# Kernel optimization log

Measured on AMD Instinct MI355X. Metric: run time of the kernel, lower is better.

Reference implementation:

```python
import jax, jax.numpy as jnp
import numpy as np

B, T, F, H, O = 64, 2048, 128, 512, 4
G = 4 * H  # gates: i, f, g, o (PyTorch order)


def setup_inputs() -> dict:
    key = jax.random.key(0)
    ks = jax.random.split(key, 12)
    s = 1.0 / np.sqrt(H)  # PyTorch LSTM init scale
    return {
        "x": jax.random.normal(ks[0], (B, T, F), dtype=jnp.float32),
        "W_ih_l0": jax.random.uniform(ks[1], (G, F), jnp.float32, -s, s),
        "W_hh_l0": jax.random.uniform(ks[2], (G, H), jnp.float32, -s, s),
        "b_ih_l0": jax.random.uniform(ks[3], (G,), jnp.float32, -s, s),
        "b_hh_l0": jax.random.uniform(ks[4], (G,), jnp.float32, -s, s),
        "W_ih_l1": jax.random.uniform(ks[5], (G, H), jnp.float32, -s, s),
        "W_hh_l1": jax.random.uniform(ks[6], (G, H), jnp.float32, -s, s),
        "b_ih_l1": jax.random.uniform(ks[7], (G,), jnp.float32, -s, s),
        "b_hh_l1": jax.random.uniform(ks[8], (G,), jnp.float32, -s, s),
        "W_out": jax.random.uniform(ks[9], (O, H), jnp.float32, -s, s),
        "b_out": jax.random.uniform(ks[10], (O,), jnp.float32, -s, s),
    }


def lstm_layer(x_seq, W_ih, W_hh, b_ih, b_hh):
    # x_seq: [B, T, Fin] -> (h_seq [B, T, H], h_final [B, H])
    b = x_seq.shape[0]
    h_dim = W_hh.shape[1]
    # Precompute input projections for all timesteps in one big GEMM.
    x_proj = jnp.einsum('btf,gf->btg', x_seq, W_ih) + b_ih + b_hh  # [B, T, 4H]

    def step(carry, xp_t):
        h, c = carry
        gates = xp_t + h @ W_hh.T  # [B, 4H]
        i, f, g, o = jnp.split(gates, 4, axis=-1)
        i = jax.nn.sigmoid(i)
        f = jax.nn.sigmoid(f)
        g = jnp.tanh(g)
        o = jax.nn.sigmoid(o)
        c = f * c + i * g
        h = o * jnp.tanh(c)
        return (h, c), h

    h0 = jnp.zeros((b, h_dim), x_seq.dtype)
    c0 = jnp.zeros((b, h_dim), x_seq.dtype)
    (hT, _), hs = jax.lax.scan(step, (h0, c0), jnp.swapaxes(x_proj, 0, 1))
    return jnp.swapaxes(hs, 0, 1), hT


def reference(x, W_ih_l0, W_hh_l0, b_ih_l0, b_hh_l0,
              W_ih_l1, W_hh_l1, b_ih_l1, b_hh_l1, W_out, b_out):
    h0_seq, h0_final = lstm_layer(x, W_ih_l0, W_hh_l0, b_ih_l0, b_hh_l0)
    _, h1_final = lstm_layer(h0_seq, W_ih_l1, W_hh_l1, b_ih_l1, b_hh_l1)
    # hn = stack([h0_final, h1_final]); relu(hn); linear applied to hn[0]
    hn0 = jax.nn.relu(h0_final)  # [B, H]
    out = hn0 @ W_out.T + b_out  # [B, 4]
    return out
```

## Files before the change

### kernel.cpp

```cpp
#include <hip/hip_runtime.h>
#include <hip/hip_bf16.h>
#include <cstdint>
#include <cstddef>


#define B_ 64
#define T_ 2048
#define F_ 128
#define H_ 512

#define NBLK 128
#define NTHR 256

#define ACT_STRIDE 1280
#define SMEM_SZ (16 * ACT_STRIDE)
#define HSLOT (B_ * H_)

typedef __bf16 bf16;
typedef __bf16 bf16x4 __attribute__((ext_vector_type(4)));
typedef __bf16 bf16x8 __attribute__((ext_vector_type(8)));
typedef float f32x4 __attribute__((ext_vector_type(4)));
typedef unsigned int u32;
typedef u32 u32x2 __attribute__((ext_vector_type(2)));
typedef u32 u32x4 __attribute__((ext_vector_type(4)));

static __device__ __forceinline__ float sigm(float v) {
  return __builtin_amdgcn_rcpf(1.f + __expf(-v));
}
static __device__ __forceinline__ float tanh_f(float v) {
  float a = fminf(fabsf(v), 20.f);
  float e = __expf(-2.f * a);
  float t = 1.f - 2.f * e * __builtin_amdgcn_rcpf(1.f + e);
  return copysignf(t, v);
}
static __device__ __forceinline__ u32 bf16bits(float f) {
  bf16 b = (bf16)f;
  unsigned short us;
  __builtin_memcpy(&us, &b, 2);
  return (u32)us;
}
static __device__ __forceinline__ u32 min4(u32x4 v) {
  u32 a = v[0] < v[1] ? v[0] : v[1];
  u32 b = v[2] < v[3] ? v[2] : v[3];
  return a < b ? a : b;
}

__global__ void __launch_bounds__(NTHR) prep_kernel(u32* hbuf) {
  int idx = blockIdx.x * blockDim.x + threadIdx.x;
  if (idx < 2 * HSLOT) hbuf[idx] = 0u;
}

__global__ void __launch_bounds__(NTHR) xconv_kernel(
    const float* __restrict__ x, bf16* __restrict__ xbf) {
  const int b = blockIdx.x;
  const int t0 = blockIdx.y * 256;
  const int f2 = threadIdx.x & 63;
  const int tq = threadIdx.x >> 6;
  const int rg = b >> 4, row = b & 15;
  for (int i = 0; i < 64; ++i) {
    int t = t0 + i * 4 + tq;
    float2 xv = *(const float2*)(x + ((size_t)b * T_ + t) * F_ + 2 * f2);
    u32 w = bf16bits(xv.x) | (bf16bits(xv.y) << 16);
    *(u32*)((char*)xbf + ((((size_t)t * 4 + rg) * 16 + row) * 128 + 2 * f2) * 2) = w;
  }
}

__global__ void __launch_bounds__(NTHR, 1) lstm_kernel(
    const float* __restrict__ x,
    const float* __restrict__ Wih,
    const float* __restrict__ Whh,
    const float* __restrict__ bih,
    const float* __restrict__ bhh,
    u32* __restrict__ hbuf,
    float* __restrict__ hf32,
    const bf16* __restrict__ xbf)
{
  __shared__ __align__(16) char smem[SMEM_SZ];

  const int tid = threadIdx.x;
  const int bid = blockIdx.x;
  const int rg = bid >> 5;
  const int jg = bid & 31;
  const int row0 = rg * 16;
  const int j0 = jg * 16;

  const int lane = tid & 63;
  const int wave = tid >> 6;
  const int fr = lane & 15;
  const int kg = lane >> 4;

  bf16x8 wfrag[20];
  {
    const int G = (fr >> 2) * H_ + j0 + wave * 4 + (fr & 3);
    const float* sih = Wih + (size_t)G * F_;
    const float* shh = Whh + (size_t)G * H_;
    #pragma unroll
    for (int kk = 0; kk < 20; ++kk) {
      const float* s = (kk < 4) ? (sih + kk * 32 + kg * 8)
                                : (shh + (kk - 4) * 32 + kg * 8);
      float4 f0 = *(const float4*)s;
      float4 f1 = *(const float4*)(s + 4);
      bf16x8 w = { (bf16)f0.x, (bf16)f0.y, (bf16)f0.z, (bf16)f0.w,
                   (bf16)f1.x, (bf16)f1.y, (bf16)f1.z, (bf16)f1.w };
      wfrag[kk] = w;
    }
  }

  const int jcol = j0 + wave * 4 + kg;
  const float bi_ = bih[0 * H_ + jcol] + bhh[0 * H_ + jcol];
  const float bf_ = bih[1 * H_ + jcol] + bhh[1 * H_ + jcol];
  const float bg_ = bih[2 * H_ + jcol] + bhh[2 * H_ + jcol];
  const float bo_ = bih[3 * H_ + jcol] + bhh[3 * H_ + jcol];

  const int prow = tid >> 4;
  const int pw = tid & 15;
  const int r0x = tid >> 5;
  const int c40 = tid & 31;
  const float* xp0 = x + (size_t)(row0 + r0x) * T_ * F_ + c40 * 4;
  const float* xp1 = x + (size_t)(row0 + r0x + 8) * T_ * F_ + c40 * 4;
  const int xw0 = r0x * ACT_STRIDE + ((8 * c40) ^ ((r0x & 7) << 4));
  const int xw1 = (r0x + 8) * ACT_STRIDE + ((8 * c40) ^ (((r0x + 8) & 7) << 4));
  const int xw = prow * ACT_STRIDE + ((pw * 16) ^ ((prow & 7) << 4));

  const char* bbase = smem + fr * ACT_STRIDE;
  const int bmask = (fr & 7) << 4;

  float c_state = 0.f;
  int budget = 1 << 22;

  for (int t = 0; t < T_; ++t) {
    if (xbf) {
      u32x4 xv = *(const u32x4*)((const char*)xbf
                  + ((size_t)t * 4 + rg) * 4096 + tid * 16);
      *(u32x4*)(smem + xw) = xv;
    } else {
      float4 xv0 = *(const float4*)(xp0 + (size_t)t * F_);
      float4 xv1 = *(const float4*)(xp1 + (size_t)t * F_);
      bf16x4 b0 = { (bf16)xv0.x, (bf16)xv0.y, (bf16)xv0.z, (bf16)xv0.w };
      bf16x4 b1 = { (bf16)xv1.x, (bf16)xv1.y, (bf16)xv1.z, (bf16)xv1.w };
      *(bf16x4*)(smem + xw0) = b0;
      *(bf16x4*)(smem + xw1) = b1;
    }
    __syncthreads();

    u32x4 v0, v1, v2, v3, v4, v5, v6, v7;
    const u32* hb = hbuf + (size_t)(t & 1) * HSLOT + (size_t)(row0 + prow) * H_ + 4 * pw;
    asm volatile("global_load_dwordx4 %0, %1, off sc0 sc1"              : "=v"(v0) : "v"(hb));
    asm volatile("global_load_dwordx4 %0, %1, off offset:256 sc0 sc1"   : "=v"(v1) : "v"(hb));
    asm volatile("global_load_dwordx4 %0, %1, off offset:512 sc0 sc1"   : "=v"(v2) : "v"(hb));
    asm volatile("global_load_dwordx4 %0, %1, off offset:768 sc0 sc1"   : "=v"(v3) : "v"(hb));
    asm volatile("global_load_dwordx4 %0, %1, off offset:1024 sc0 sc1"  : "=v"(v4) : "v"(hb));
    asm volatile("global_load_dwordx4 %0, %1, off offset:1280 sc0 sc1"  : "=v"(v5) : "v"(hb));
    asm volatile("global_load_dwordx4 %0, %1, off offset:1536 sc0 sc1"  : "=v"(v6) : "v"(hb));
    asm volatile("global_load_dwordx4 %0, %1, off offset:1792 sc0 sc1"  : "=v"(v7) : "v"(hb));
    __builtin_amdgcn_sched_barrier(0);

    f32x4 a0 = {0.f, 0.f, 0.f, 0.f}, a1 = {0.f, 0.f, 0.f, 0.f};
    f32x4 a2 = {0.f, 0.f, 0.f, 0.f}, a3 = {0.f, 0.f, 0.f, 0.f};
    {
      bf16x8 p0 = *(const bf16x8*)(bbase + ((0 * 64 + kg * 16) ^ bmask));
      a0 = __builtin_amdgcn_mfma_f32_16x16x32_bf16(wfrag[0], p0, a0, 0, 0, 0);
      bf16x8 p1 = *(const bf16x8*)(bbase + ((1 * 64 + kg * 16) ^ bmask));
      a1 = __builtin_amdgcn_mfma_f32_16x16x32_bf16(wfrag[1], p1, a1, 0, 0, 0);
      bf16x8 p2 = *(const bf16x8*)(bbase + ((2 * 64 + kg * 16) ^ bmask));
      a2 = __builtin_amdgcn_mfma_f32_16x16x32_bf16(wfrag[2], p2, a2, 0, 0, 0);
      bf16x8 p3 = *(const bf16x8*)(bbase + ((3 * 64 + kg * 16) ^ bmask));
      a3 = __builtin_amdgcn_mfma_f32_16x16x32_bf16(wfrag[3], p3, a3, 0, 0, 0);
    }
    __builtin_amdgcn_sched_barrier(0);

    {
      const u32 tgt = (u32)t << 16;
      for (;;) {
        asm volatile("s_waitcnt vmcnt(0)" ::: "memory");
        __builtin_amdgcn_sched_barrier(0);
        u32 need = 0;
        if (min4(v0) < tgt) need |= 1u;
        if (min4(v1) < tgt) need |= 2u;
        if (min4(v2) < tgt) need |= 4u;
        if (min4(v3) < tgt) need |= 8u;
        if (min4(v4) < tgt) need |= 16u;
        if (min4(v5) < tgt) need |= 32u;
        if (min4(v6) < tgt) need |= 64u;
        if (min4(v7) < tgt) need |= 128u;
        if (!need) break;
        if (--budget < 0) break;
        if (need & 1u)   asm volatile("global_load_dwordx4 %0, %1, off sc0 sc1"             : "=v"(v0) : "v"(hb));
        if (need & 2u)   asm volatile("global_load_dwordx4 %0, %1, off offset:256 sc0 sc1"  : "=v"(v1) : "v"(hb));
        if (need & 4u)   asm volatile("global_load_dwordx4 %0, %1, off offset:512 sc0 sc1"  : "=v"(v2) : "v"(hb));
        if (need & 8u)   asm volatile("global_load_dwordx4 %0, %1, off offset:768 sc0 sc1"  : "=v"(v3) : "v"(hb));
        if (need & 16u)  asm volatile("global_load_dwordx4 %0, %1, off offset:1024 sc0 sc1" : "=v"(v4) : "v"(hb));
        if (need & 32u)  asm volatile("global_load_dwordx4 %0, %1, off offset:1280 sc0 sc1" : "=v"(v5) : "v"(hb));
        if (need & 64u)  asm volatile("global_load_dwordx4 %0, %1, off offset:1536 sc0 sc1" : "=v"(v6) : "v"(hb));
        if (need & 128u) asm volatile("global_load_dwordx4 %0, %1, off offset:1792 sc0 sc1" : "=v"(v7) : "v"(hb));
      }
    }

    {
      char* dst = smem + prow * ACT_STRIDE;
      const int swz = (prow & 7) << 4;
      #define UNPACK(i, V)                                                  \
        {                                                                   \
          u32 w0 = (V[0] & 0xffffu) | (V[1] << 16);                         \
          u32 w1 = (V[2] & 0xffffu) | (V[3] << 16);                         \
          u32x2 wp = { w0, w1 };                                            \
          *(u32x2*)(dst + ((256 + 128 * (i) + 8 * pw) ^ swz)) = wp;         \
        }
      UNPACK(0, v0) UNPACK(1, v1) UNPACK(2, v2) UNPACK(3, v3)
      UNPACK(4, v4) UNPACK(5, v5) UNPACK(6, v6) UNPACK(7, v7)
      #undef UNPACK
    }
    __syncthreads();

    #pragma unroll
    for (int kk = 4; kk < 20; kk += 4) {
      bf16x8 b0 = *(const bf16x8*)(bbase + (((kk + 0) * 64 + kg * 16) ^ bmask));
      a0 = __builtin_amdgcn_mfma_f32_16x16x32_bf16(wfrag[kk + 0], b0, a0, 0, 0, 0);
      bf16x8 b1 = *(const bf16x8*)(bbase + (((kk + 1) * 64 + kg * 16) ^ bmask));
      a1 = __builtin_amdgcn_mfma_f32_16x16x32_bf16(wfrag[kk + 1], b1, a1, 0, 0, 0);
      bf16x8 b2 = *(const bf16x8*)(bbase + (((kk + 2) * 64 + kg * 16) ^ bmask));
      a2 = __builtin_amdgcn_mfma_f32_16x16x32_bf16(wfrag[kk + 2], b2, a2, 0, 0, 0);
      bf16x8 b3 = *(const bf16x8*)(bbase + (((kk + 3) * 64 + kg * 16) ^ bmask));
      a3 = __builtin_amdgcn_mfma_f32_16x16x32_bf16(wfrag[kk + 3], b3, a3, 0, 0, 0);
    }
    f32x4 dsum = (a0 + a1) + (a2 + a3);

    float d0 = dsum[0], d1 = dsum[1], d2 = dsum[2], d3 = dsum[3];
    float t0 = __shfl_xor((kg & 2) ? d0 : d2, 32, 64);
    float t1 = __shfl_xor((kg & 2) ? d1 : d3, 32, 64);
    float w0 = (kg & 2) ? t0 : d0;
    float w1 = (kg & 2) ? t1 : d1;
    float w2 = (kg & 2) ? d2 : t0;
    float w3 = (kg & 2) ? d3 : t1;
    float t2 = __shfl_xor((kg & 1) ? w0 : w1, 16, 64);
    float t3 = __shfl_xor((kg & 1) ? w2 : w3, 16, 64);
    float gi = (kg & 1) ? t2 : w0;
    float gf = (kg & 1) ? w1 : t2;
    float gg = (kg & 1) ? t3 : w2;
    float go = (kg & 1) ? w3 : t3;

    float iv = sigm(gi + bi_);
    float fv = sigm(gf + bf_);
    float gv = tanh_f(gg + bg_);
    float ov = sigm(go + bo_);
    c_state = fv * c_state + iv * gv;
    float hv = ov * tanh_f(c_state);

    u32 val = ((u32)(t + 1) << 16) | bf16bits(hv);
    u32* dstp = hbuf + (size_t)((t + 1) & 1) * HSLOT + (size_t)(row0 + fr) * H_ + jcol;
    asm volatile("global_atomic_swap %0, %1, off" :: "v"(dstp), "v"(val) : "memory");

    if (t == T_ - 1) hf32[(size_t)(row0 + fr) * H_ + jcol] = hv;
  }
}

__global__ void __launch_bounds__(64) out_kernel(
    const float* __restrict__ h_f32,
    const float* __restrict__ Wout,
    const float* __restrict__ bout,
    float* __restrict__ out)
{
  int b = blockIdx.x;
  int lane = threadIdx.x;
  float a0 = 0.f, a1 = 0.f, a2 = 0.f, a3 = 0.f;
  for (int j = lane; j < H_; j += 64) {
    float hv = fmaxf(h_f32[(size_t)b * H_ + j], 0.f);
    a0 += hv * Wout[0 * H_ + j];
    a1 += hv * Wout[1 * H_ + j];
    a2 += hv * Wout[2 * H_ + j];
    a3 += hv * Wout[3 * H_ + j];
  }
  #pragma unroll
  for (int off = 32; off; off >>= 1) {
    a0 += __shfl_down(a0, off);
    a1 += __shfl_down(a1, off);
    a2 += __shfl_down(a2, off);
    a3 += __shfl_down(a3, off);
  }
  if (lane == 0) {
    out[b * 4 + 0] = a0 + bout[0];
    out[b * 4 + 1] = a1 + bout[1];
    out[b * 4 + 2] = a2 + bout[2];
    out[b * 4 + 3] = a3 + bout[3];
  }
}

extern "C" void kernel_launch(void* const* d_in, const int* in_sizes, int n_in,
                              void* d_out, int out_size, void* d_ws, size_t ws_size,
                              hipStream_t stream) {
  const float* x    = (const float*)d_in[0];
  const float* Wih  = (const float*)d_in[1];
  const float* Whh  = (const float*)d_in[2];
  const float* bih  = (const float*)d_in[3];
  const float* bhh  = (const float*)d_in[4];
  const float* Wout = (const float*)d_in[9];
  const float* bout = (const float*)d_in[10];

  char* ws = (char*)d_ws;
  u32*   hbuf = (u32*)ws;
  float* hf32 = (float*)(ws + 262144);
  const size_t XBF_OFF = 393216;
  const size_t XBF_SZ = (size_t)T_ * 4 * 16 * 128 * 2;
  bf16* xbf = (ws_size >= XBF_OFF + XBF_SZ) ? (bf16*)(ws + XBF_OFF) : nullptr;

  hipLaunchKernelGGL(prep_kernel, dim3(256), dim3(NTHR), 0, stream, hbuf);
  if (xbf)
    hipLaunchKernelGGL(xconv_kernel, dim3(64, 8), dim3(NTHR), 0, stream, x, xbf);

  void* args[] = { (void*)&x, (void*)&Wih, (void*)&Whh, (void*)&bih, (void*)&bhh,
                   (void*)&hbuf, (void*)&hf32, (void*)&xbf };
  hipLaunchCooperativeKernel((void*)lstm_kernel, dim3(NBLK), dim3(NTHR),
                             args, 0, stream);

  hipLaunchKernelGGL(out_kernel, dim3(B_), dim3(64), 0, stream,
                     hf32, Wout, bout, (float*)d_out);
}
```

Measured before the change: 3.925 ms.

## Use 32 cooperative blocks of 1024 threads instead of 128 of 256

```diff
diff --git a/kernel.cpp b/kernel.cpp
--- a/kernel.cpp
+++ b/kernel.cpp
@@ -9,8 +9,8 @@
 #define F_ 128
 #define H_ 512
 
-#define NBLK 128
-#define NTHR 256
+#define NBLK 32
+#define NTHR 1024
 
 #define ACT_STRIDE 1280
 #define SMEM_SZ (16 * ACT_STRIDE)
@@ -21,7 +21,6 @@
 typedef __bf16 bf16x8 __attribute__((ext_vector_type(8)));
 typedef float f32x4 __attribute__((ext_vector_type(4)));
 typedef unsigned int u32;
-typedef u32 u32x2 __attribute__((ext_vector_type(2)));
 typedef u32 u32x4 __attribute__((ext_vector_type(4)));
 
 static __device__ __forceinline__ float sigm(float v) {
@@ -45,12 +44,12 @@
   return a < b ? a : b;
 }
 
-__global__ void __launch_bounds__(NTHR) prep_kernel(u32* hbuf) {
+__global__ void __launch_bounds__(256) prep_kernel(u32* hbuf) {
   int idx = blockIdx.x * blockDim.x + threadIdx.x;
   if (idx < 2 * HSLOT) hbuf[idx] = 0u;
 }
 
-__global__ void __launch_bounds__(NTHR) xconv_kernel(
+__global__ void __launch_bounds__(256) xconv_kernel(
     const float* __restrict__ x, bf16* __restrict__ xbf) {
   const int b = blockIdx.x;
   const int t0 = blockIdx.y * 256;
@@ -79,10 +78,10 @@
 
   const int tid = threadIdx.x;
   const int bid = blockIdx.x;
-  const int rg = bid >> 5;
-  const int jg = bid & 31;
+  const int rg = bid >> 3;
+  const int jg = bid & 7;
   const int row0 = rg * 16;
-  const int j0 = jg * 16;
+  const int j0 = jg * 64;
 
   const int lane = tid & 63;
   const int wave = tid >> 6;
@@ -112,16 +111,9 @@
   const float bg_ = bih[2 * H_ + jcol] + bhh[2 * H_ + jcol];
   const float bo_ = bih[3 * H_ + jcol] + bhh[3 * H_ + jcol];
 
-  const int prow = tid >> 4;
-  const int pw = tid & 15;
-  const int r0x = tid >> 5;
-  const int c40 = tid & 31;
-  const float* xp0 = x + (size_t)(row0 + r0x) * T_ * F_ + c40 * 4;
-  const float* xp1 = x + (size_t)(row0 + r0x + 8) * T_ * F_ + c40 * 4;
-  const int xw0 = r0x * ACT_STRIDE + ((8 * c40) ^ ((r0x & 7) << 4));
-  const int xw1 = (r0x + 8) * ACT_STRIDE + ((8 * c40) ^ (((r0x + 8) & 7) << 4));
-  const int xw = prow * ACT_STRIDE + ((pw * 16) ^ ((prow & 7) << 4));
-
+  const int prow = tid >> 6;
+  const int pw = tid & 63;
+  const int swz = (prow & 7) << 4;
   const char* bbase = smem + fr * ACT_STRIDE;
   const int bmask = (fr & 7) << 4;
 
@@ -130,29 +122,20 @@
 
   for (int t = 0; t < T_; ++t) {
     if (xbf) {
-      u32x4 xv = *(const u32x4*)((const char*)xbf
-                  + ((size_t)t * 4 + rg) * 4096 + tid * 16);
-      *(u32x4*)(smem + xw) = xv;
+      u32 xv = *(const u32*)((const char*)xbf
+                + ((size_t)t * 4 + rg) * 4096 + tid * 4);
+      *(u32*)(smem + prow * ACT_STRIDE + ((4 * pw) ^ swz)) = xv;
     } else {
-      float4 xv0 = *(const float4*)(xp0 + (size_t)t * F_);
-      float4 xv1 = *(const float4*)(xp1 + (size_t)t * F_);
-      bf16x4 b0 = { (bf16)xv0.x, (bf16)xv0.y, (bf16)xv0.z, (bf16)xv0.w };
-      bf16x4 b1 = { (bf16)xv1.x, (bf16)xv1.y, (bf16)xv1.z, (bf16)xv1.w };
-      *(bf16x4*)(smem + xw0) = b0;
-      *(bf16x4*)(smem + xw1) = b1;
+      float2 xv = *(const float2*)(x + ((size_t)(row0 + prow) * T_ + t) * F_ + 2 * pw);
+      u32 w = bf16bits(xv.x) | (bf16bits(xv.y) << 16);
+      *(u32*)(smem + prow * ACT_STRIDE + ((4 * pw) ^ swz)) = w;
     }
     __syncthreads();
 
-    u32x4 v0, v1, v2, v3, v4, v5, v6, v7;
-    const u32* hb = hbuf + (size_t)(t & 1) * HSLOT + (size_t)(row0 + prow) * H_ + 4 * pw;
-    asm volatile("global_load_dwordx4 %0, %1, off sc0 sc1"              : "=v"(v0) : "v"(hb));
-    asm volatile("global_load_dwordx4 %0, %1, off offset:256 sc0 sc1"   : "=v"(v1) : "v"(hb));
-    asm volatile("global_load_dwordx4 %0, %1, off offset:512 sc0 sc1"   : "=v"(v2) : "v"(hb));
-    asm volatile("global_load_dwordx4 %0, %1, off offset:768 sc0 sc1"   : "=v"(v3) : "v"(hb));
-    asm volatile("global_load_dwordx4 %0, %1, off offset:1024 sc0 sc1"  : "=v"(v4) : "v"(hb));
-    asm volatile("global_load_dwordx4 %0, %1, off offset:1280 sc0 sc1"  : "=v"(v5) : "v"(hb));
-    asm volatile("global_load_dwordx4 %0, %1, off offset:1536 sc0 sc1"  : "=v"(v6) : "v"(hb));
-    asm volatile("global_load_dwordx4 %0, %1, off offset:1792 sc0 sc1"  : "=v"(v7) : "v"(hb));
+    u32x4 v0, v1;
+    const u32* hb = hbuf + (size_t)(t & 1) * HSLOT + (size_t)(row0 + prow) * H_ + 8 * pw;
+    asm volatile("global_load_dwordx4 %0, %1, off sc0 sc1"            : "=v"(v0) : "v"(hb));
+    asm volatile("global_load_dwordx4 %0, %1, off offset:16 sc0 sc1"  : "=v"(v1) : "v"(hb));
     __builtin_amdgcn_sched_barrier(0);
 
     f32x4 a0 = {0.f, 0.f, 0.f, 0.f}, a1 = {0.f, 0.f, 0.f, 0.f};
@@ -177,38 +160,19 @@
         u32 need = 0;
         if (min4(v0) < tgt) need |= 1u;
         if (min4(v1) < tgt) need |= 2u;
-        if (min4(v2) < tgt) need |= 4u;
-        if (min4(v3) < tgt) need |= 8u;
-        if (min4(v4) < tgt) need |= 16u;
-        if (min4(v5) < tgt) need |= 32u;
-        if (min4(v6) < tgt) need |= 64u;
-        if (min4(v7) < tgt) need |= 128u;
         if (!need) break;
         if (--budget < 0) break;
-        if (need & 1u)   asm volatile("global_load_dwordx4 %0, %1, off sc0 sc1"             : "=v"(v0) : "v"(hb));
-        if (need & 2u)   asm volatile("global_load_dwordx4 %0, %1, off offset:256 sc0 sc1"  : "=v"(v1) : "v"(hb));
-        if (need & 4u)   asm volatile("global_load_dwordx4 %0, %1, off offset:512 sc0 sc1"  : "=v"(v2) : "v"(hb));
-        if (need & 8u)   asm volatile("global_load_dwordx4 %0, %1, off offset:768 sc0 sc1"  : "=v"(v3) : "v"(hb));
-        if (need & 16u)  asm volatile("global_load_dwordx4 %0, %1, off offset:1024 sc0 sc1" : "=v"(v4) : "v"(hb));
-        if (need & 32u)  asm volatile("global_load_dwordx4 %0, %1, off offset:1280 sc0 sc1" : "=v"(v5) : "v"(hb));
-        if (need & 64u)  asm volatile("global_load_dwordx4 %0, %1, off offset:1536 sc0 sc1" : "=v"(v6) : "v"(hb));
-        if (need & 128u) asm volatile("global_load_dwordx4 %0, %1, off offset:1792 sc0 sc1" : "=v"(v7) : "v"(hb));
+        if (need & 1u) asm volatile("global_load_dwordx4 %0, %1, off sc0 sc1"           : "=v"(v0) : "v"(hb));
+        if (need & 2u) asm volatile("global_load_dwordx4 %0, %1, off offset:16 sc0 sc1" : "=v"(v1) : "v"(hb));
       }
     }
 
     {
-      char* dst = smem + prow * ACT_STRIDE;
-      const int swz = (prow & 7) << 4;
-      #define UNPACK(i, V)                                                  \
-        {                                                                   \
-          u32 w0 = (V[0] & 0xffffu) | (V[1] << 16);                         \
-          u32 w1 = (V[2] & 0xffffu) | (V[3] << 16);                         \
-          u32x2 wp = { w0, w1 };                                            \
-          *(u32x2*)(dst + ((256 + 128 * (i) + 8 * pw) ^ swz)) = wp;         \
-        }
-      UNPACK(0, v0) UNPACK(1, v1) UNPACK(2, v2) UNPACK(3, v3)
-      UNPACK(4, v4) UNPACK(5, v5) UNPACK(6, v6) UNPACK(7, v7)
-      #undef UNPACK
+      u32x4 w = { (v0[0] & 0xffffu) | (v0[1] << 16),
+                  (v0[2] & 0xffffu) | (v0[3] << 16),
+                  (v1[0] & 0xffffu) | (v1[1] << 16),
+                  (v1[2] & 0xffffu) | (v1[3] << 16) };
+      *(u32x4*)(smem + prow * ACT_STRIDE + ((256 + 16 * pw) ^ swz)) = w;
     }
     __syncthreads();
 
@@ -303,9 +267,9 @@
   const size_t XBF_SZ = (size_t)T_ * 4 * 16 * 128 * 2;
   bf16* xbf = (ws_size >= XBF_OFF + XBF_SZ) ? (bf16*)(ws + XBF_OFF) : nullptr;
 
-  hipLaunchKernelGGL(prep_kernel, dim3(256), dim3(NTHR), 0, stream, hbuf);
+  hipLaunchKernelGGL(prep_kernel, dim3(256), dim3(256), 0, stream, hbuf);
   if (xbf)
-    hipLaunchKernelGGL(xconv_kernel, dim3(64, 8), dim3(NTHR), 0, stream, x, xbf);
+    hipLaunchKernelGGL(xconv_kernel, dim3(64, 8), dim3(256), 0, stream, x, xbf);
 
   void* args[] = { (void*)&x, (void*)&Wih, (void*)&Whh, (void*)&bih, (void*)&bhh,
                    (void*)&hbuf, (void*)&hf32, (void*)&xbf };
```

Measured after the change: 8.339 ms. 2.12x slower.
